# Kernel optimization log

Measured on AMD Instinct MI355X. Metric: run time of the kernel, lower is better.

Reference implementation:

```python
import jax, jax.numpy as jnp
import numpy as np

MAX_DISP = 48
PATCH = 3
OFFSET = 0
PAD = PATCH // 2
EPS = 1e-3


def _unfold(x, P, pad):
    # x: [B,C,H,W] -> [B,C,K2,H,W], K2 enumerated row-major over the PxP window
    B, C, H, W = x.shape
    xp = jnp.pad(x, ((0, 0), (0, 0), (pad, pad), (pad, pad)))
    return jnp.stack([xp[:, :, i:i + H, j:j + W]
                      for i in range(P) for j in range(P)], axis=2)


def _normalize(x, axes):
    # torch F.normalize: x / clamp(||x||_2, min=eps)
    n = jnp.sqrt(jnp.sum(x * x, axis=axes, keepdims=True))
    return x / jnp.maximum(n, EPS)


def setup_inputs() -> dict:
    key = jax.random.key(0)
    k1, k2, k3 = jax.random.split(key, 3)
    shp = (2, 32, 128, 416)
    return {
        "xl": jax.random.normal(k1, shp, dtype=jnp.float32),
        "xm": jax.random.normal(k2, shp, dtype=jnp.float32),
        "xr": jax.random.normal(k3, shp, dtype=jnp.float32),
    }


def reference(xl, xm, xr):
    B, C, H, W = xl.shape
    K2 = PATCH * PATCH
    scale = (C * K2) ** 0.5

    pl = _normalize(_unfold(xl, PATCH, PAD), (1, 2))  # [B,C,K2,H,W]
    pr = _normalize(_unfold(xr, PATCH, PAD), (1, 2))
    fl = _normalize(xm, (1,))                          # [B,C,H,W]

    # fl is constant over the K2 axis, so sum patches over K2 once for sim_L/sim_R
    Sl = pl.sum(axis=2)  # [B,C,H,W]
    Sr = pr.sum(axis=2)

    cL, cR, cLR = [], [], []
    for d in range(OFFSET, OFFSET + MAX_DISP):
        if d > 0:
            # shifted_l[w] = patches_l[w+d] (zero right pad); shifted_r[w] = patches_r[w-d]
            sL = jnp.einsum('bchw,bchw->bhw', fl[..., :W - d], Sl[..., d:])
            sL = jnp.pad(sL, ((0, 0), (0, 0), (0, d)))
            sR = jnp.einsum('bchw,bchw->bhw', fl[..., d:], Sr[..., :W - d])
            sR = jnp.pad(sR, ((0, 0), (0, 0), (d, 0)))
            wlr = W - 2 * d  # overlap region of the two opposite shifts
            if wlr > 0:
                sLR = jnp.einsum('bckhw,bckhw->bhw', pl[..., 2 * d:], pr[..., :wlr])
                sLR = jnp.pad(sLR, ((0, 0), (0, 0), (d, d)))
            else:
                sLR = jnp.zeros((B, H, W), xl.dtype)
        else:
            sL = jnp.einsum('bchw,bchw->bhw', fl, Sl)
            sR = jnp.einsum('bchw,bchw->bhw', fl, Sr)
            sLR = jnp.einsum('bckhw,bckhw->bhw', pl, pr)
        cL.append(sL / scale)
        cR.append(sR / scale)
        cLR.append(sLR / scale)

    cost = jnp.stack([jnp.stack(cL, 1), jnp.stack(cR, 1), jnp.stack(cLR, 1)], axis=1)
    return jnp.clip(cost, -10.0, 10.0).astype(jnp.float16)  # [B,3,D,H,W]
```

## Files before the change

### kernel.cpp

```cpp
#include <hip/hip_runtime.h>
#include <math.h>

#define B 2
#define C 32
#define H 128
#define W 416
#define D 48
#define HW (H*W)
#define CHW (C*HW)
#define EPSN 1e-3f
#define ISCALE 0.05892556509887896f
#define LSTR 36
#define DSPL (D / 2)

__device__ __forceinline__ float clip10(float x) {
    return fminf(fmaxf(x, -10.0f), 10.0f);
}

__global__ __launch_bounds__(256) void k_norm(const float* __restrict__ sql,
                                              const float* __restrict__ sqr,
                                              float* __restrict__ inl,
                                              float* __restrict__ inr) {
    int idx = blockIdx.x * 256 + threadIdx.x;
    if (idx >= B * HW) return;
    int b = idx / HW, hw = idx - b * HW;
    int h = hw / W, w = hw - h * W;
    float sl = 0.f, sr = 0.f;
#pragma unroll
    for (int di = -1; di <= 1; ++di) {
        int hh = h + di;
        if (hh < 0 || hh >= H) continue;
#pragma unroll
        for (int dj = -1; dj <= 1; ++dj) {
            int ww = w + dj;
            if (ww < 0 || ww >= W) continue;
            int p = b * HW + hh * W + ww;
            sl += sql[p];
            sr += sqr[p];
        }
    }
    inl[idx] = 1.0f / fmaxf(sqrtf(sl), EPSN);
    inr[idx] = 1.0f / fmaxf(sqrtf(sr), EPSN);
}

__device__ __forceinline__ void stage_row_v2(const float* __restrict__ gsrc,
                                             float* __restrict__ lds,
                                             int tid, int nthreads) {
    for (int t = tid; t < (W / 4) * C; t += nthreads) {
        int rw = t & 7;
        int cl = (t >> 3) & 7;
        int g  = t >> 6;
        int wg = g % 13;
        int ch = g / 13;
        int c  = ch * 8 + cl;
        int w4 = (wg * 8 + rw) * 4;
        float4 v = *(const float4*)(gsrc + (size_t)c * HW + w4);
        lds[(w4 + 0) * LSTR + c] = v.x;
        lds[(w4 + 1) * LSTR + c] = v.y;
        lds[(w4 + 2) * LSTR + c] = v.z;
        lds[(w4 + 3) * LSTR + c] = v.w;
    }
}

__device__ __forceinline__ void stage_row3_v2(const float* __restrict__ gsrc,
                                              float* __restrict__ lds,
                                              int h, int tid, int nthreads) {
    for (int t = tid; t < (W / 4) * C; t += nthreads) {
        int rw = t & 7;
        int cl = (t >> 3) & 7;
        int g  = t >> 6;
        int wg = g % 13;
        int ch = g / 13;
        int c  = ch * 8 + cl;
        int w4 = (wg * 8 + rw) * 4;
        const float* p = gsrc + (size_t)c * HW + w4;
        float4 v = *(const float4*)(p);
        if (h > 0) {
            float4 a = *(const float4*)(p - W);
            v.x += a.x; v.y += a.y; v.z += a.z; v.w += a.w;
        }
        if (h < H - 1) {
            float4 a = *(const float4*)(p + W);
            v.x += a.x; v.y += a.y; v.z += a.z; v.w += a.w;
        }
        lds[(w4 + 0) * LSTR + c] = v.x;
        lds[(w4 + 1) * LSTR + c] = v.y;
        lds[(w4 + 2) * LSTR + c] = v.z;
        lds[(w4 + 3) * LSTR + c] = v.w;
    }
}

__device__ __forceinline__ float dot32(const float* __restrict__ fl,
                                       const float* __restrict__ col) {
    const float4* c4 = (const float4*)col;
    float a = 0.0f;
#pragma unroll
    for (int q = 0; q < 8; ++q) {
        float4 v = c4[q];
        a += fl[4 * q + 0] * v.x + fl[4 * q + 1] * v.y
           + fl[4 * q + 2] * v.z + fl[4 * q + 3] * v.w;
    }
    return a;
}

__device__ __forceinline__ void dot32x2(const float* __restrict__ fl0,
                                        const float* __restrict__ fl1,
                                        const float* __restrict__ col,
                                        float& a0, float& a1) {
    const float4* c4 = (const float4*)col;
    float s0 = 0.f, s1 = 0.f;
#pragma unroll
    for (int q = 0; q < 8; ++q) {
        float4 v = c4[q];
        s0 += fl0[4 * q + 0] * v.x + fl0[4 * q + 1] * v.y
            + fl0[4 * q + 2] * v.z + fl0[4 * q + 3] * v.w;
        s1 += fl1[4 * q + 0] * v.x + fl1[4 * q + 1] * v.y
            + fl1[4 * q + 2] * v.z + fl1[4 * q + 3] * v.w;
    }
    a0 = s0; a1 = s1;
}

__global__ __launch_bounds__(256) void k_lr(const float* __restrict__ xm,
                                            const float* __restrict__ xl,
                                            const float* __restrict__ xr,
                                            const float* __restrict__ inl,
                                            const float* __restrict__ inr,
                                            float* __restrict__ out) {
    __shared__ float sB[W * LSTR];
    __shared__ float sIn[W];
    int tid = threadIdx.x;
    int h = blockIdx.x;
    int b = blockIdx.y;
    int d0 = blockIdx.z * DSPL;
    bool act = tid < (W / 2);
    int w = 2 * tid;
    int bhw = b * HW + h * W;
    const float* pm = xm + (size_t)b * CHW + h * W;

    float fl0[C], fl1[C];
    if (act) {
        float am0 = 0.f, am1 = 0.f;
#pragma unroll
        for (int c = 0; c < C; ++c) {
            float2 mv = *(const float2*)(pm + c * HW + w);
            fl0[c] = mv.x; fl1[c] = mv.y;
            am0 += mv.x * mv.x; am1 += mv.y * mv.y;
        }
        float im0 = 1.0f / fmaxf(sqrtf(am0), EPSN);
        float im1 = 1.0f / fmaxf(sqrtf(am1), EPSN);
#pragma unroll
        for (int c = 0; c < C; ++c) { fl0[c] *= im0; fl1[c] *= im1; }
    } else {
#pragma unroll
        for (int c = 0; c < C; ++c) { fl0[c] = 0.f; fl1[c] = 0.f; }
    }

    stage_row3_v2(xl + (size_t)b * CHW + h * W, sB, h, tid, 256);
    for (int j = tid; j < W; j += 256) sIn[j] = inl[bhw + j];
    __syncthreads();
    if (act) {
        float* o = out + ((size_t)b * 3 + 0) * D * HW + h * W;
        float g0a = 0.f, g0b = 0.f, g1a = 0.f, g1b = 0.f, s0p = 0.f;
#pragma unroll 4
        for (int j = 0; j <= DSPL + 2; ++j) {
            int v = w + d0 - 1 + j;
            float c0 = 0.f, c1 = 0.f;
            if (v >= 0 && v < W) dot32x2(fl0, fl1, sB + v * LSTR, c0, c1);
            float s0 = 0.f, s1 = 0.f;
            if (j >= 2) {
                int m = v - 1;
                if (m < W) {
                    float sc = sIn[m] * ISCALE;
                    s0 = clip10((g0a + g0b + c0) * sc);
                    s1 = clip10((g1a + g1b + c1) * sc);
                }
                if (j >= 3) {
                    int d = d0 + j - 3;
                    *(float2*)(o + (size_t)d * HW + w) = make_float2(s0p, s1);
                }
            }
            s0p = s0;
            g0a = g0b; g0b = c0;
            g1a = g1b; g1b = c1;
        }
    }
    __syncthreads();

    stage_row3_v2(xr + (size_t)b * CHW + h * W, sB, h, tid, 256);
    for (int j = tid; j < W; j += 256) sIn[j] = inr[bhw + j];
    __syncthreads();
    if (act) {
        float* o = out + ((size_t)b * 3 + 1) * D * HW + h * W;
        float g0a = 0.f, g0b = 0.f, g1a = 0.f, g1b = 0.f, s0p = 0.f;
#pragma unroll 4
        for (int j = 0; j <= DSPL + 2; ++j) {
            int v = w - d0 - DSPL + j;
            float c0 = 0.f, c1 = 0.f;
            if (v >= 0 && v < W) dot32x2(fl0, fl1, sB + v * LSTR, c0, c1);
            float s0 = 0.f, s1 = 0.f;
            if (j >= 2) {
                int m = v - 1;
                if (m >= 0) {
                    float sc = sIn[m] * ISCALE;
                    s0 = clip10((g0a + g0b + c0) * sc);
                    s1 = clip10((g1a + g1b + c1) * sc);
                }
                if (j >= 3) {
                    int d = d0 + DSPL + 2 - j;
                    *(float2*)(o + (size_t)d * HW + w) = make_float2(s0p, s1);
                }
            }
            s0p = s0;
            g0a = g0b; g0b = c0;
            g1a = g1b; g1b = c1;
        }
    }
}

__global__ __launch_bounds__(448) void k_e(const float* __restrict__ xl,
                                           const float* __restrict__ xr,
                                           float* __restrict__ EH,
                                           float* __restrict__ sql,
                                           float* __restrict__ sqr) {
    __shared__ float sXL[W * LSTR];
    int tid = threadIdx.x;
    int h = blockIdx.x;
    int b = blockIdx.y;
    int d0 = blockIdx.z * DSPL;
    int lane = tid & 63;
    int wv = tid >> 6;
    int v = wv * 62 + lane - 1;
    bool vin = (v >= 0) && (v < W);
    const float* br = xr + (size_t)b * CHW + h * W;

    float xrv[C];
#pragma unroll
    for (int c = 0; c < C; ++c) xrv[c] = vin ? br[c * HW + v] : 0.0f;

    stage_row_v2(xl + (size_t)b * CHW + h * W, sXL, tid, 448);
    __syncthreads();

    bool wr = (lane >= 1) && (lane <= 62) && (v < W);

    if (blockIdx.z == 0) {
        float sr_ = 0.f, sl_ = 0.f;
#pragma unroll
        for (int c = 0; c < C; ++c) sr_ += xrv[c] * xrv[c];
        if (vin) {
            const float4* c4 = (const float4*)(sXL + v * LSTR);
#pragma unroll
            for (int q = 0; q < 8; ++q) {
                float4 x = c4[q];
                sl_ += x.x * x.x + x.y * x.y + x.z * x.z + x.w * x.w;
            }
        }
        if (wr) {
            sqr[b * HW + h * W + v] = sr_;
            sql[b * HW + h * W + v] = sl_;
        }
    }

    float* pe = EH + (((size_t)b * D) * H + h) * W + v;
    for (int d = d0; d < d0 + DSPL; ++d) {
        int s = 2 * d;
        float e = 0.0f;
        if (vin && v + s < W) e = dot32(xrv, sXL + (v + s) * LSTR);
        float em = __shfl_up(e, 1);
        float ep = __shfl_down(e, 1);
        float eh = em + e + ep;
        if (wr) pe[(size_t)d * HW] = eh;
    }
}

#define DCH 12
__global__ __launch_bounds__(448) void k_lr2(const float* __restrict__ EH,
                                             const float* __restrict__ inl,
                                             const float* __restrict__ inr,
                                             float* __restrict__ out) {
    int w = threadIdx.x;
    int dc = blockIdx.x;
    int h = blockIdx.y;
    int b = blockIdx.z;
    if (w >= W) return;
    int bhw = b * HW + h * W;
    bool hm = (h > 0), hp = (h < H - 1);

    float* o = out + ((size_t)b * 3 + 2) * D * HW + h * W + w;
#pragma unroll
    for (int i = 0; i < DCH; ++i) {
        int d = dc * DCH + i;
        float r = 0.0f;
        if (w >= d && w + d < W) {
            int vc = w - d;
            const float* base = EH + ((size_t)b * D + d) * HW + vc;
            float e = base[h * W];
            if (hm) e += base[(h - 1) * W];
            if (hp) e += base[(h + 1) * W];
            float nl = inl[bhw + w + d];
            float nr = inr[bhw + vc];
            r = clip10(e * nl * nr * ISCALE);
        }
        o[(size_t)d * HW] = r;
    }
}

extern "C" void kernel_launch(void* const* d_in, const int* in_sizes, int n_in,
                              void* d_out, int out_size, void* d_ws, size_t ws_size,
                              hipStream_t stream) {
    const float* xl = (const float*)d_in[0];
    const float* xm = (const float*)d_in[1];
    const float* xr = (const float*)d_in[2];
    float* out = (float*)d_out;

    float* ws = (float*)d_ws;
    float* inl = ws;
    float* inr = inl + B * HW;
    float* sql = inr + B * HW;
    float* sqr = sql + B * HW;
    float* EH  = sqr + B * HW;

    k_e<<<dim3(H, B, 2), dim3(448), 0, stream>>>(xl, xr, EH, sql, sqr);
    k_norm<<<dim3((B * HW + 255) / 256), dim3(256), 0, stream>>>(sql, sqr, inl, inr);
    k_lr<<<dim3(H, B, 2), dim3(256), 0, stream>>>(xm, xl, xr, inl, inr, out);
    k_lr2<<<dim3(4, H, B), dim3(448), 0, stream>>>(EH, inl, inr, out);
}
```

Baseline: 164.6 us.

## Split disparity range across thread halves and swizzle LDS layout in k_lr

k_lr now runs 448 threads per block, with each pair of threads splitting its 24-disparity chunk into two halves of 12. The block's shared tile uses an XOR swizzle on float4 groups so that neighbouring columns read from different LDS banks. k_e doubles its block size to 896 and splits its disparity loop between two thread halves in the same way. The aim is more parallelism per row and fewer LDS bank conflicts. The cost is redundant fl/xrv register loads per thread, higher register pressure at the larger launch bounds, and each half redoing the 2-disparity warmup of the sliding window.

```diff
diff --git a/kernel.cpp b/kernel.cpp
--- a/kernel.cpp
+++ b/kernel.cpp
@@ -12,6 +12,8 @@
 #define ISCALE 0.05892556509887896f
 #define LSTR 36
 #define DSPL (D / 2)
+#define DHALF (DSPL / 2)
+#define SWZ(v) (((v) >> 1) & 7)
 
 __device__ __forceinline__ float clip10(float x) {
     return fminf(fmaxf(x, -10.0f), 10.0f);
@@ -62,9 +64,9 @@
     }
 }
 
-__device__ __forceinline__ void stage_row3_v2(const float* __restrict__ gsrc,
-                                              float* __restrict__ lds,
-                                              int h, int tid, int nthreads) {
+__device__ __forceinline__ void stage_row3_swz(const float* __restrict__ gsrc,
+                                               float* __restrict__ lds,
+                                               int h, int tid, int nthreads) {
     for (int t = tid; t < (W / 4) * C; t += nthreads) {
         int rw = t & 7;
         int cl = (t >> 3) & 7;
@@ -83,10 +85,13 @@
             float4 a = *(const float4*)(p + W);
             v.x += a.x; v.y += a.y; v.z += a.z; v.w += a.w;
         }
-        lds[(w4 + 0) * LSTR + c] = v.x;
-        lds[(w4 + 1) * LSTR + c] = v.y;
-        lds[(w4 + 2) * LSTR + c] = v.z;
-        lds[(w4 + 3) * LSTR + c] = v.w;
+        int g2 = c >> 2, wd = c & 3;
+        int sA = SWZ(w4);
+        int sB_ = (sA + 1) & 7;
+        lds[(w4 + 0) * LSTR + 4 * (g2 ^ sA) + wd] = v.x;
+        lds[(w4 + 1) * LSTR + 4 * (g2 ^ sA) + wd] = v.y;
+        lds[(w4 + 2) * LSTR + 4 * (g2 ^ sB_) + wd] = v.z;
+        lds[(w4 + 3) * LSTR + 4 * (g2 ^ sB_) + wd] = v.w;
     }
 }
 
@@ -103,15 +108,15 @@
     return a;
 }
 
-__device__ __forceinline__ void dot32x2(const float* __restrict__ fl0,
-                                        const float* __restrict__ fl1,
-                                        const float* __restrict__ col,
-                                        float& a0, float& a1) {
+__device__ __forceinline__ void dot32x2s(const float* __restrict__ fl0,
+                                         const float* __restrict__ fl1,
+                                         const float* __restrict__ col, int s,
+                                         float& a0, float& a1) {
     const float4* c4 = (const float4*)col;
     float s0 = 0.f, s1 = 0.f;
 #pragma unroll
     for (int q = 0; q < 8; ++q) {
-        float4 v = c4[q];
+        float4 v = c4[q ^ s];
         s0 += fl0[4 * q + 0] * v.x + fl0[4 * q + 1] * v.y
             + fl0[4 * q + 2] * v.z + fl0[4 * q + 3] * v.w;
         s1 += fl1[4 * q + 0] * v.x + fl1[4 * q + 1] * v.y
@@ -120,7 +125,7 @@
     a0 = s0; a1 = s1;
 }
 
-__global__ __launch_bounds__(256) void k_lr(const float* __restrict__ xm,
+__global__ __launch_bounds__(448) void k_lr(const float* __restrict__ xm,
                                             const float* __restrict__ xl,
                                             const float* __restrict__ xr,
                                             const float* __restrict__ inl,
@@ -132,8 +137,11 @@
     int h = blockIdx.x;
     int b = blockIdx.y;
     int d0 = blockIdx.z * DSPL;
-    bool act = tid < (W / 2);
-    int w = 2 * tid;
+    bool act = tid < W;
+    int p = tid >> 1;
+    int half = tid & 1;
+    int w = 2 * p;
+    int dbase = d0 + half * DHALF;
     int bhw = b * HW + h * W;
     const float* pm = xm + (size_t)b * CHW + h * W;
 
@@ -155,17 +163,17 @@
         for (int c = 0; c < C; ++c) { fl0[c] = 0.f; fl1[c] = 0.f; }
     }
 
-    stage_row3_v2(xl + (size_t)b * CHW + h * W, sB, h, tid, 256);
-    for (int j = tid; j < W; j += 256) sIn[j] = inl[bhw + j];
+    stage_row3_swz(xl + (size_t)b * CHW + h * W, sB, h, tid, 448);
+    for (int j = tid; j < W; j += 448) sIn[j] = inl[bhw + j];
     __syncthreads();
     if (act) {
         float* o = out + ((size_t)b * 3 + 0) * D * HW + h * W;
         float g0a = 0.f, g0b = 0.f, g1a = 0.f, g1b = 0.f, s0p = 0.f;
-#pragma unroll 4
-        for (int j = 0; j <= DSPL + 2; ++j) {
-            int v = w + d0 - 1 + j;
+#pragma unroll 3
+        for (int j = 0; j <= DHALF + 2; ++j) {
+            int v = w + dbase - 1 + j;
             float c0 = 0.f, c1 = 0.f;
-            if (v >= 0 && v < W) dot32x2(fl0, fl1, sB + v * LSTR, c0, c1);
+            if (v >= 0 && v < W) dot32x2s(fl0, fl1, sB + v * LSTR, SWZ(v), c0, c1);
             float s0 = 0.f, s1 = 0.f;
             if (j >= 2) {
                 int m = v - 1;
@@ -175,7 +183,7 @@
                     s1 = clip10((g1a + g1b + c1) * sc);
                 }
                 if (j >= 3) {
-                    int d = d0 + j - 3;
+                    int d = dbase + j - 3;
                     *(float2*)(o + (size_t)d * HW + w) = make_float2(s0p, s1);
                 }
             }
@@ -186,17 +194,17 @@
     }
     __syncthreads();
 
-    stage_row3_v2(xr + (size_t)b * CHW + h * W, sB, h, tid, 256);
-    for (int j = tid; j < W; j += 256) sIn[j] = inr[bhw + j];
+    stage_row3_swz(xr + (size_t)b * CHW + h * W, sB, h, tid, 448);
+    for (int j = tid; j < W; j += 448) sIn[j] = inr[bhw + j];
     __syncthreads();
     if (act) {
         float* o = out + ((size_t)b * 3 + 1) * D * HW + h * W;
         float g0a = 0.f, g0b = 0.f, g1a = 0.f, g1b = 0.f, s0p = 0.f;
-#pragma unroll 4
-        for (int j = 0; j <= DSPL + 2; ++j) {
-            int v = w - d0 - DSPL + j;
+#pragma unroll 3
+        for (int j = 0; j <= DHALF + 2; ++j) {
+            int v = w - dbase - DHALF + j;
             float c0 = 0.f, c1 = 0.f;
-            if (v >= 0 && v < W) dot32x2(fl0, fl1, sB + v * LSTR, c0, c1);
+            if (v >= 0 && v < W) dot32x2s(fl0, fl1, sB + v * LSTR, SWZ(v), c0, c1);
             float s0 = 0.f, s1 = 0.f;
             if (j >= 2) {
                 int m = v - 1;
@@ -206,7 +214,7 @@
                     s1 = clip10((g1a + g1b + c1) * sc);
                 }
                 if (j >= 3) {
-                    int d = d0 + DSPL + 2 - j;
+                    int d = dbase + DHALF + 2 - j;
                     *(float2*)(o + (size_t)d * HW + w) = make_float2(s0p, s1);
                 }
             }
@@ -217,7 +225,7 @@
     }
 }
 
-__global__ __launch_bounds__(448) void k_e(const float* __restrict__ xl,
+__global__ __launch_bounds__(896) void k_e(const float* __restrict__ xl,
                                            const float* __restrict__ xr,
                                            float* __restrict__ EH,
                                            float* __restrict__ sql,
@@ -229,7 +237,9 @@
     int d0 = blockIdx.z * DSPL;
     int lane = tid & 63;
     int wv = tid >> 6;
-    int v = wv * 62 + lane - 1;
+    int half = (wv >= 7) ? 1 : 0;
+    int wv7 = wv - 7 * half;
+    int v = wv7 * 62 + lane - 1;
     bool vin = (v >= 0) && (v < W);
     const float* br = xr + (size_t)b * CHW + h * W;
 
@@ -237,12 +247,12 @@
 #pragma unroll
     for (int c = 0; c < C; ++c) xrv[c] = vin ? br[c * HW + v] : 0.0f;
 
-    stage_row_v2(xl + (size_t)b * CHW + h * W, sXL, tid, 448);
+    stage_row_v2(xl + (size_t)b * CHW + h * W, sXL, tid, 896);
     __syncthreads();
 
     bool wr = (lane >= 1) && (lane <= 62) && (v < W);
 
-    if (blockIdx.z == 0) {
+    if (blockIdx.z == 0 && half == 0) {
         float sr_ = 0.f, sl_ = 0.f;
 #pragma unroll
         for (int c = 0; c < C; ++c) sr_ += xrv[c] * xrv[c];
@@ -261,7 +271,8 @@
     }
 
     float* pe = EH + (((size_t)b * D) * H + h) * W + v;
-    for (int d = d0; d < d0 + DSPL; ++d) {
+    int dlo = d0 + half * DHALF;
+    for (int d = dlo; d < dlo + DHALF; ++d) {
         int s = 2 * d;
         float e = 0.0f;
         if (vin && v + s < W) e = dot32(xrv, sXL + (v + s) * LSTR);
@@ -319,8 +330,8 @@
     float* sqr = sql + B * HW;
     float* EH  = sqr + B * HW;
 
-    k_e<<<dim3(H, B, 2), dim3(448), 0, stream>>>(xl, xr, EH, sql, sqr);
+    k_e<<<dim3(H, B, 2), dim3(896), 0, stream>>>(xl, xr, EH, sql, sqr);
     k_norm<<<dim3((B * HW + 255) / 256), dim3(256), 0, stream>>>(sql, sqr, inl, inr);
-    k_lr<<<dim3(H, B, 2), dim3(256), 0, stream>>>(xm, xl, xr, inl, inr, out);
+    k_lr<<<dim3(H, B, 2), dim3(448), 0, stream>>>(xm, xl, xr, inl, inr, out);
     k_lr2<<<dim3(4, H, B), dim3(448), 0, stream>>>(EH, inl, inr, out);
 }
```

Result: slower. 183.1 us (+11.3%).

## Swizzle LDS layout in k_lr, split disparities three ways, drop sIn staging

Applied to the files above, without the earlier changes.

k_lr now stores staged rows with a 32-float stride and an XOR swizzle on float4 groups, replacing the padded 36-float stride. The goal is to cut LDS footprint and bank conflicts, which should allow three blocks per CU (launch_bounds 256,3). Disparities are split into three chunks of 16 per row with a flattened grid. The per-row inverse-norm buffer in shared memory is dropped in favour of prefetched global loads, and the dot products get branchless clamped indexing with split accumulators. Trade-off: each chunk restages the xl/xr rows (three times instead of twice) and adds extra halo work per chunk.

```diff
diff --git a/kernel.cpp b/kernel.cpp
--- a/kernel.cpp
+++ b/kernel.cpp
@@ -10,12 +10,18 @@
 #define CHW (C*HW)
 #define EPSN 1e-3f
 #define ISCALE 0.05892556509887896f
-#define LSTR 36
-#define DSPL (D / 2)
+#define ESTR 36
+#define LSTR 32
+#define DSPE 24
+#define DSPL 16
+#define NZ 3
 
 __device__ __forceinline__ float clip10(float x) {
     return fminf(fmaxf(x, -10.0f), 10.0f);
 }
+
+#define FMA4(acc, f, k, u) acc += f[4*(k)+0]*(u).x + f[4*(k)+1]*(u).y \
+                               + f[4*(k)+2]*(u).z + f[4*(k)+3]*(u).w;
 
 __global__ __launch_bounds__(256) void k_norm(const float* __restrict__ sql,
                                               const float* __restrict__ sqr,
@@ -55,16 +61,16 @@
         int c  = ch * 8 + cl;
         int w4 = (wg * 8 + rw) * 4;
         float4 v = *(const float4*)(gsrc + (size_t)c * HW + w4);
-        lds[(w4 + 0) * LSTR + c] = v.x;
-        lds[(w4 + 1) * LSTR + c] = v.y;
-        lds[(w4 + 2) * LSTR + c] = v.z;
-        lds[(w4 + 3) * LSTR + c] = v.w;
-    }
-}
-
-__device__ __forceinline__ void stage_row3_v2(const float* __restrict__ gsrc,
-                                              float* __restrict__ lds,
-                                              int h, int tid, int nthreads) {
+        lds[(w4 + 0) * ESTR + c] = v.x;
+        lds[(w4 + 1) * ESTR + c] = v.y;
+        lds[(w4 + 2) * ESTR + c] = v.z;
+        lds[(w4 + 3) * ESTR + c] = v.w;
+    }
+}
+
+__device__ __forceinline__ void stage_row3_swz(const float* __restrict__ gsrc,
+                                               float* __restrict__ lds,
+                                               int h, int tid, int nthreads) {
     for (int t = tid; t < (W / 4) * C; t += nthreads) {
         int rw = t & 7;
         int cl = (t >> 3) & 7;
@@ -83,55 +89,54 @@
             float4 a = *(const float4*)(p + W);
             v.x += a.x; v.y += a.y; v.z += a.z; v.w += a.w;
         }
-        lds[(w4 + 0) * LSTR + c] = v.x;
-        lds[(w4 + 1) * LSTR + c] = v.y;
-        lds[(w4 + 2) * LSTR + c] = v.z;
-        lds[(w4 + 3) * LSTR + c] = v.w;
-    }
-}
-
-__device__ __forceinline__ float dot32(const float* __restrict__ fl,
-                                       const float* __restrict__ col) {
+        int g2 = c >> 2, wd = c & 3;
+        int k0 = (w4 >> 1) & 7;
+        int k1 = (k0 + 1) & 7;
+        lds[(w4 + 0) * LSTR + 4 * (g2 ^ k0) + wd] = v.x;
+        lds[(w4 + 1) * LSTR + 4 * (g2 ^ k0) + wd] = v.y;
+        lds[(w4 + 2) * LSTR + 4 * (g2 ^ k1) + wd] = v.z;
+        lds[(w4 + 3) * LSTR + 4 * (g2 ^ k1) + wd] = v.w;
+    }
+}
+
+__device__ __forceinline__ float dot32e(const float* __restrict__ x,
+                                        const float* __restrict__ col) {
     const float4* c4 = (const float4*)col;
-    float a = 0.0f;
-#pragma unroll
-    for (int q = 0; q < 8; ++q) {
-        float4 v = c4[q];
-        a += fl[4 * q + 0] * v.x + fl[4 * q + 1] * v.y
-           + fl[4 * q + 2] * v.z + fl[4 * q + 3] * v.w;
-    }
-    return a;
-}
-
-__device__ __forceinline__ void dot32x2(const float* __restrict__ fl0,
-                                        const float* __restrict__ fl1,
-                                        const float* __restrict__ col,
-                                        float& a0, float& a1) {
-    const float4* c4 = (const float4*)col;
-    float s0 = 0.f, s1 = 0.f;
-#pragma unroll
-    for (int q = 0; q < 8; ++q) {
-        float4 v = c4[q];
-        s0 += fl0[4 * q + 0] * v.x + fl0[4 * q + 1] * v.y
-            + fl0[4 * q + 2] * v.z + fl0[4 * q + 3] * v.w;
-        s1 += fl1[4 * q + 0] * v.x + fl1[4 * q + 1] * v.y
-            + fl1[4 * q + 2] * v.z + fl1[4 * q + 3] * v.w;
-    }
-    a0 = s0; a1 = s1;
-}
-
-__global__ __launch_bounds__(256) void k_lr(const float* __restrict__ xm,
-                                            const float* __restrict__ xl,
-                                            const float* __restrict__ xr,
-                                            const float* __restrict__ inl,
-                                            const float* __restrict__ inr,
-                                            float* __restrict__ out) {
+    float4 u0 = c4[0], u1 = c4[1], u2 = c4[2], u3 = c4[3];
+    float4 u4 = c4[4], u5 = c4[5], u6 = c4[6], u7 = c4[7];
+    float a = 0.f, b = 0.f;
+    FMA4(a, x, 0, u0) FMA4(a, x, 1, u1) FMA4(a, x, 2, u2) FMA4(a, x, 3, u3)
+    FMA4(b, x, 4, u4) FMA4(b, x, 5, u5) FMA4(b, x, 6, u6) FMA4(b, x, 7, u7)
+    return a + b;
+}
+
+__device__ __forceinline__ void dot2s(const float* __restrict__ fl0,
+                                      const float* __restrict__ fl1,
+                                      const float4* __restrict__ c4, int ky,
+                                      float& a0, float& a1) {
+    float4 u0 = c4[ky],     u1 = c4[1 ^ ky], u2 = c4[2 ^ ky], u3 = c4[3 ^ ky];
+    float4 u4 = c4[4 ^ ky], u5 = c4[5 ^ ky], u6 = c4[6 ^ ky], u7 = c4[7 ^ ky];
+    float x0 = 0.f, x1 = 0.f, y0 = 0.f, y1 = 0.f;
+    FMA4(x0, fl0, 0, u0) FMA4(x0, fl0, 1, u1) FMA4(x0, fl0, 2, u2) FMA4(x0, fl0, 3, u3)
+    FMA4(x1, fl0, 4, u4) FMA4(x1, fl0, 5, u5) FMA4(x1, fl0, 6, u6) FMA4(x1, fl0, 7, u7)
+    FMA4(y0, fl1, 0, u0) FMA4(y0, fl1, 1, u1) FMA4(y0, fl1, 2, u2) FMA4(y0, fl1, 3, u3)
+    FMA4(y1, fl1, 4, u4) FMA4(y1, fl1, 5, u5) FMA4(y1, fl1, 6, u6) FMA4(y1, fl1, 7, u7)
+    a0 = x0 + x1; a1 = y0 + y1;
+}
+
+__global__ __launch_bounds__(256, 3) void k_lr(const float* __restrict__ xm,
+                                               const float* __restrict__ xl,
+                                               const float* __restrict__ xr,
+                                               const float* __restrict__ inl,
+                                               const float* __restrict__ inr,
+                                               float* __restrict__ out) {
     __shared__ float sB[W * LSTR];
-    __shared__ float sIn[W];
     int tid = threadIdx.x;
-    int h = blockIdx.x;
+    int bx = blockIdx.x;
+    int z = bx % NZ;
+    int h = bx / NZ;
     int b = blockIdx.y;
-    int d0 = blockIdx.z * DSPL;
+    int d0 = z * DSPL;
     bool act = tid < (W / 2);
     int w = 2 * tid;
     int bhw = b * HW + h * W;
@@ -142,7 +147,7 @@
         float am0 = 0.f, am1 = 0.f;
 #pragma unroll
         for (int c = 0; c < C; ++c) {
-            float2 mv = *(const float2*)(pm + c * HW + w);
+            float2 mv = *(const float2*)(pm + (size_t)c * HW + w);
             fl0[c] = mv.x; fl1[c] = mv.y;
             am0 += mv.x * mv.x; am1 += mv.y * mv.y;
         }
@@ -150,29 +155,33 @@
         float im1 = 1.0f / fmaxf(sqrtf(am1), EPSN);
 #pragma unroll
         for (int c = 0; c < C; ++c) { fl0[c] *= im0; fl1[c] *= im1; }
-    } else {
-#pragma unroll
-        for (int c = 0; c < C; ++c) { fl0[c] = 0.f; fl1[c] = 0.f; }
-    }
-
-    stage_row3_v2(xl + (size_t)b * CHW + h * W, sB, h, tid, 256);
-    for (int j = tid; j < W; j += 256) sIn[j] = inl[bhw + j];
+    }
+
+    stage_row3_swz(xl + (size_t)b * CHW + h * W, sB, h, tid, 256);
     __syncthreads();
     if (act) {
         float* o = out + ((size_t)b * 3 + 0) * D * HW + h * W;
+        const float* inx = inl + bhw;
         float g0a = 0.f, g0b = 0.f, g1a = 0.f, g1b = 0.f, s0p = 0.f;
-#pragma unroll 4
+        float scn = 0.f;
         for (int j = 0; j <= DSPL + 2; ++j) {
             int v = w + d0 - 1 + j;
-            float c0 = 0.f, c1 = 0.f;
-            if (v >= 0 && v < W) dot32x2(fl0, fl1, sB + v * LSTR, c0, c1);
+            bool ok = (v >= 0) && (v < W);
+            int vc = ok ? v : 0;
+            float c0, c1;
+            dot2s(fl0, fl1, (const float4*)(sB + vc * LSTR), (vc >> 1) & 7, c0, c1);
+            c0 = ok ? c0 : 0.f;
+            c1 = ok ? c1 : 0.f;
+            float sc = scn;
+            int mn = w + d0 + j - 1;
+            scn = (mn >= 0 && mn < W) ? inx[mn] : 0.f;
             float s0 = 0.f, s1 = 0.f;
             if (j >= 2) {
                 int m = v - 1;
                 if (m < W) {
-                    float sc = sIn[m] * ISCALE;
-                    s0 = clip10((g0a + g0b + c0) * sc);
-                    s1 = clip10((g1a + g1b + c1) * sc);
+                    float s = sc * ISCALE;
+                    s0 = clip10((g0a + g0b + c0) * s);
+                    s1 = clip10((g1a + g1b + c1) * s);
                 }
                 if (j >= 3) {
                     int d = d0 + j - 3;
@@ -186,24 +195,31 @@
     }
     __syncthreads();
 
-    stage_row3_v2(xr + (size_t)b * CHW + h * W, sB, h, tid, 256);
-    for (int j = tid; j < W; j += 256) sIn[j] = inr[bhw + j];
+    stage_row3_swz(xr + (size_t)b * CHW + h * W, sB, h, tid, 256);
     __syncthreads();
     if (act) {
         float* o = out + ((size_t)b * 3 + 1) * D * HW + h * W;
+        const float* inx = inr + bhw;
         float g0a = 0.f, g0b = 0.f, g1a = 0.f, g1b = 0.f, s0p = 0.f;
-#pragma unroll 4
+        float scn = 0.f;
         for (int j = 0; j <= DSPL + 2; ++j) {
             int v = w - d0 - DSPL + j;
-            float c0 = 0.f, c1 = 0.f;
-            if (v >= 0 && v < W) dot32x2(fl0, fl1, sB + v * LSTR, c0, c1);
+            bool ok = (v >= 0) && (v < W);
+            int vc = ok ? v : 0;
+            float c0, c1;
+            dot2s(fl0, fl1, (const float4*)(sB + vc * LSTR), (vc >> 1) & 7, c0, c1);
+            c0 = ok ? c0 : 0.f;
+            c1 = ok ? c1 : 0.f;
+            float sc = scn;
+            int mn = w - d0 - DSPL + j;
+            scn = (mn >= 0) ? inx[mn] : 0.f;
             float s0 = 0.f, s1 = 0.f;
             if (j >= 2) {
                 int m = v - 1;
                 if (m >= 0) {
-                    float sc = sIn[m] * ISCALE;
-                    s0 = clip10((g0a + g0b + c0) * sc);
-                    s1 = clip10((g1a + g1b + c1) * sc);
+                    float s = sc * ISCALE;
+                    s0 = clip10((g0a + g0b + c0) * s);
+                    s1 = clip10((g1a + g1b + c1) * s);
                 }
                 if (j >= 3) {
                     int d = d0 + DSPL + 2 - j;
@@ -222,11 +238,11 @@
                                            float* __restrict__ EH,
                                            float* __restrict__ sql,
                                            float* __restrict__ sqr) {
-    __shared__ float sXL[W * LSTR];
+    __shared__ float sXL[W * ESTR];
     int tid = threadIdx.x;
     int h = blockIdx.x;
     int b = blockIdx.y;
-    int d0 = blockIdx.z * DSPL;
+    int d0 = blockIdx.z * DSPE;
     int lane = tid & 63;
     int wv = tid >> 6;
     int v = wv * 62 + lane - 1;
@@ -247,7 +263,7 @@
 #pragma unroll
         for (int c = 0; c < C; ++c) sr_ += xrv[c] * xrv[c];
         if (vin) {
-            const float4* c4 = (const float4*)(sXL + v * LSTR);
+            const float4* c4 = (const float4*)(sXL + v * ESTR);
 #pragma unroll
             for (int q = 0; q < 8; ++q) {
                 float4 x = c4[q];
@@ -261,10 +277,10 @@
     }
 
     float* pe = EH + (((size_t)b * D) * H + h) * W + v;
-    for (int d = d0; d < d0 + DSPL; ++d) {
+    for (int d = d0; d < d0 + DSPE; ++d) {
         int s = 2 * d;
         float e = 0.0f;
-        if (vin && v + s < W) e = dot32(xrv, sXL + (v + s) * LSTR);
+        if (vin && v + s < W) e = dot32e(xrv, sXL + (v + s) * ESTR);
         float em = __shfl_up(e, 1);
         float ep = __shfl_down(e, 1);
         float eh = em + e + ep;
@@ -321,6 +337,6 @@
 
     k_e<<<dim3(H, B, 2), dim3(448), 0, stream>>>(xl, xr, EH, sql, sqr);
     k_norm<<<dim3((B * HW + 255) / 256), dim3(256), 0, stream>>>(sql, sqr, inl, inr);
-    k_lr<<<dim3(H, B, 2), dim3(256), 0, stream>>>(xm, xl, xr, inl, inr, out);
+    k_lr<<<dim3(NZ * H, B), dim3(256), 0, stream>>>(xm, xl, xr, inl, inr, out);
     k_lr2<<<dim3(4, H, B), dim3(448), 0, stream>>>(EH, inl, inr, out);
 }
```

New measurement: 195.5 us. 18.8% more time.
